# Kernel tuning notes

Measured on AMD Instinct MI355X. Metric: run time of the kernel, lower is better.

Reference implementation:

```python
import jax, jax.numpy as jnp
import numpy as np

S, B, D, E, F = 2048, 2, 1024, 8, 4096


def setup_inputs() -> dict:
    key = jax.random.key(0)
    ks = jax.random.split(key, 6)
    x = jax.random.normal(ks[0], (S, B, D), dtype=jnp.float32)
    w_switch = jax.random.normal(ks[1], (D, E), dtype=jnp.float32) / np.sqrt(D)
    b_switch = jnp.zeros((E,), dtype=jnp.float32)
    w1 = jax.random.normal(ks[2], (E, D, F), dtype=jnp.float32) / np.sqrt(D)
    b1 = jnp.zeros((E, F), dtype=jnp.float32)
    w2 = jax.random.normal(ks[3], (E, F, D), dtype=jnp.float32) / np.sqrt(F)
    b2 = jnp.zeros((E, D), dtype=jnp.float32)
    return {"x": x, "w_switch": w_switch, "b_switch": b_switch,
            "w1": w1, "b1": b1, "w2": w2, "b2": b2}


def reference(x, w_switch, b_switch, w1, b1, w2, b2):
    # x: [S, B, D] -> tokens [N, D]
    s, b, d = x.shape
    n_experts = w1.shape[0]
    xf = x.reshape(-1, d)                                    # [N, D]
    route_prob = jax.nn.softmax(xf @ w_switch + b_switch, axis=-1)  # [N, E]
    route_prob_max = jnp.max(route_prob, axis=-1)            # [N]
    routes = jnp.argmax(route_prob, axis=-1)                 # [N] int
    # is_scale_prob=True: scale token by its routing probability before FFN
    xs = xf * route_prob_max[:, None]                        # [N, D]
    # Per-expert FFN evaluated densely (drop_tokens=False => every token kept),
    # then each token selects its routed expert's output.
    h = jax.nn.relu(jnp.einsum('nd,edf->enf', xs, w1) + b1[:, None, :])  # [E, N, F]
    y = jnp.einsum('enf,efd->end', h, w2) + b2[:, None, :]               # [E, N, D]
    n = xf.shape[0]
    out = y[routes, jnp.arange(n)]                           # [N, D]
    counts = jnp.zeros((n_experts,), dtype=jnp.float32).at[routes].add(1.0)
    n_dropped = jnp.zeros((), dtype=jnp.int32)               # drop_tokens=False
    return out.reshape(s, b, d), counts, route_prob.sum(0), n_dropped
```

## Files before the change

### kernel.cpp

```cpp
#include <hip/hip_runtime.h>
#include <hip/hip_bf16.h>

#define NTOK 4096
#define DDIM 1024
#define NEXP 8
#define FDIM 4096

typedef __attribute__((ext_vector_type(4))) float f32x4;
typedef __attribute__((ext_vector_type(8))) short bf16x8;
typedef __attribute__((ext_vector_type(8))) unsigned short u16x8;

#define GLDS(g, l) __builtin_amdgcn_global_load_lds( \
    (const __attribute__((address_space(1))) unsigned int*)(g), \
    (__attribute__((address_space(3))) unsigned int*)(l), 16, 0, 0)

__global__ __launch_bounds__(256) void route_kernel(
    const float* __restrict__ x,
    const float* __restrict__ w_switch,
    const float* __restrict__ b_switch,
    __hip_bfloat16* __restrict__ xs,
    int* __restrict__ amax_arr,
    float* __restrict__ partial)
{
    const int tid = threadIdx.x;
    const int wave = tid >> 6, lane = tid & 63;
    __shared__ float pr[4][16];

    float wacc[16];
#pragma unroll
    for (int j = 0; j < 16; j++) wacc[j] = 0.0f;

    for (int i = 0; i < 4; i++) {
        const int n = blockIdx.x * 16 + wave * 4 + i;
        const float4* xr = (const float4*)(x + (size_t)n * DDIM);
        float4 xv[4];
#pragma unroll
        for (int j = 0; j < 4; j++) xv[j] = xr[lane + j * 64];

        float acc[NEXP];
#pragma unroll
        for (int e = 0; e < NEXP; e++) acc[e] = 0.0f;
#pragma unroll
        for (int j = 0; j < 4; j++) {
            const int dbase = (lane + j * 64) * 4;
#pragma unroll
            for (int c = 0; c < 4; c++) {
                const float4* wr = (const float4*)(w_switch + (size_t)(dbase + c) * NEXP);
                float4 w0 = wr[0], w1 = wr[1];
                float xvc = ((const float*)&xv[j])[c];
                acc[0] += xvc * w0.x; acc[1] += xvc * w0.y;
                acc[2] += xvc * w0.z; acc[3] += xvc * w0.w;
                acc[4] += xvc * w1.x; acc[5] += xvc * w1.y;
                acc[6] += xvc * w1.z; acc[7] += xvc * w1.w;
            }
        }
#pragma unroll
        for (int e = 0; e < NEXP; e++) {
            float v = acc[e];
#pragma unroll
            for (int off = 32; off > 0; off >>= 1) v += __shfl_xor(v, off, 64);
            acc[e] = v;
        }
        float mx = -1e30f;
#pragma unroll
        for (int e = 0; e < NEXP; e++) {
            acc[e] += b_switch[e];
            mx = fmaxf(mx, acc[e]);
        }
        float sum = 0.0f;
#pragma unroll
        for (int e = 0; e < NEXP; e++) { acc[e] = __expf(acc[e] - mx); sum += acc[e]; }
        float inv = 1.0f / sum;
        float pmax = -1.0f; int amax = 0;
#pragma unroll
        for (int e = 0; e < NEXP; e++) {
            float p = acc[e] * inv;
            acc[e] = p;
            if (p > pmax) { pmax = p; amax = e; }
        }
#pragma unroll
        for (int e = 0; e < NEXP; e++) {
            wacc[e] += acc[e];
            wacc[8 + e] += (amax == e) ? 1.0f : 0.0f;
        }
        if (lane == 0) amax_arr[n] = amax;
#pragma unroll
        for (int j = 0; j < 4; j++) {
            ushort4 pk;
            __hip_bfloat16* pp = (__hip_bfloat16*)&pk;
            pp[0] = __float2bfloat16(xv[j].x * pmax);
            pp[1] = __float2bfloat16(xv[j].y * pmax);
            pp[2] = __float2bfloat16(xv[j].z * pmax);
            pp[3] = __float2bfloat16(xv[j].w * pmax);
            *(ushort4*)(xs + (size_t)n * DDIM + (lane + j * 64) * 4) = pk;
        }
    }
    if (lane == 0) {
#pragma unroll
        for (int j = 0; j < 16; j++) pr[wave][j] = wacc[j];
    }
    __syncthreads();
    if (tid < 16)
        partial[blockIdx.x * 16 + tid] = pr[0][tid] + pr[1][tid] + pr[2][tid] + pr[3][tid];
}

__global__ __launch_bounds__(256) void finalize_kernel(
    const float* __restrict__ partial, float* __restrict__ out_tail)
{
    __shared__ float red[16][16];
    const int j = threadIdx.x & 15, g = threadIdx.x >> 4;
    float s = 0.0f;
    for (int k = 0; k < 16; k++) s += partial[(size_t)(g + k * 16) * 16 + j];
    red[g][j] = s;
    __syncthreads();
    if (threadIdx.x < 16) {
        float t = 0.0f;
        for (int k = 0; k < 16; k++) t += red[k][threadIdx.x];
        int dst = (threadIdx.x < 8) ? (8 + threadIdx.x) : (threadIdx.x - 8);
        out_tail[dst] = t;
    }
    if (threadIdx.x == 16) out_tail[16] = 0.0f;
}

__global__ __launch_bounds__(1024) void bucket_kernel(
    const int* __restrict__ amax_arr, int* __restrict__ bucket, int* __restrict__ ecnt)
{
    const int e = blockIdx.x;
    __shared__ int ctr;
    if (threadIdx.x == 0) ctr = 0;
    __syncthreads();
    const int lane = threadIdx.x & 63;
    for (int c = 0; c < NTOK; c += 1024) {
        int t = c + threadIdx.x;
        bool my = (amax_arr[t] == e);
        unsigned long long mask = __ballot(my);
        int cnt = __popcll(mask);
        int base = 0;
        if (lane == 0 && cnt) base = atomicAdd(&ctr, cnt);
        base = __shfl(base, 0, 64);
        if (my) {
            int rank = __popcll(mask & ((1ull << lane) - 1ull));
            bucket[e * NTOK + base + rank] = t;
        }
    }
    __syncthreads();
    if (threadIdx.x == 0) ecnt[e] = ctr;
}

template <int R, int C>
__global__ __launch_bounds__(256) void transpose_kernel(
    const float* __restrict__ in, __hip_bfloat16* __restrict__ outp)
{
    const int e = blockIdx.z;
    const int r0 = blockIdx.y * 64, c0 = blockIdx.x * 64;
    __shared__ __hip_bfloat16 t[64 * 65];
    const int tid = threadIdx.x;
    const int ri = tid >> 4, c4 = (tid & 15) * 4;
    const float* src = in + ((size_t)e * R + r0) * C + c0;
#pragma unroll
    for (int rr = 0; rr < 4; rr++) {
        int r = ri + rr * 16;
        float4 v = *(const float4*)(src + (size_t)r * C + c4);
        t[r * 65 + c4 + 0] = __float2bfloat16(v.x);
        t[r * 65 + c4 + 1] = __float2bfloat16(v.y);
        t[r * 65 + c4 + 2] = __float2bfloat16(v.z);
        t[r * 65 + c4 + 3] = __float2bfloat16(v.w);
    }
    __syncthreads();
    const int co = tid >> 2, m = tid & 3;
    u16x8 v0, v1;
#pragma unroll
    for (int idx = 0; idx < 8; idx++)
        ((unsigned short*)&v0)[idx] = *(const unsigned short*)&t[(m * 16 + idx) * 65 + co];
#pragma unroll
    for (int idx = 0; idx < 8; idx++)
        ((unsigned short*)&v1)[idx] = *(const unsigned short*)&t[(m * 16 + idx + 8) * 65 + co];
    __hip_bfloat16* dst = outp + ((size_t)e * C + c0 + co) * R + r0 + m * 16;
    *(u16x8*)(dst) = v0;
    *(u16x8*)(dst + 8) = v1;
}

template <int MODE, int K, int NN>
__global__ __launch_bounds__(256) void gemm_kernel(
    const __hip_bfloat16* __restrict__ A,
    const __hip_bfloat16* __restrict__ Bt,
    const float* __restrict__ bias,
    const int* __restrict__ bucket,
    const int* __restrict__ ecnt,
    void* __restrict__ Out)
{
    const int e = blockIdx.z;
    const int cnt = ecnt[e];
    const int m0 = blockIdx.y * 128;
    if (m0 >= cnt) return;
    const int n0 = blockIdx.x * 128;

    __shared__ __align__(16) __hip_bfloat16 Asm[128 * 32];
    __shared__ __align__(16) __hip_bfloat16 Bsm[128 * 32];
    __shared__ int toks[128];

    const int tid = threadIdx.x;
    if (tid < 128) {
        int r = m0 + tid;
        toks[tid] = bucket[e * NTOK + (r < cnt ? r : cnt - 1)];
    }
    __syncthreads();

    const int wave = tid >> 6, lane = tid & 63;
    const int r = lane & 15, kq = lane >> 4;
    const int g0 = 2 * wave, g1 = 2 * wave + 1;

    const __hip_bfloat16* pA0 = A + (size_t)toks[g0 * 16 + r] * K + kq * 8;
    const __hip_bfloat16* pA1 = A + (size_t)toks[g1 * 16 + r] * K + kq * 8;
    const __hip_bfloat16* pB0 = Bt + ((size_t)e * NN + n0 + g0 * 16 + r) * K + kq * 8;
    const __hip_bfloat16* pB1 = Bt + ((size_t)e * NN + n0 + g1 * 16 + r) * K + kq * 8;
    char* lA0 = (char*)Asm + g0 * 1024;
    char* lA1 = (char*)Asm + g1 * 1024;
    char* lB0 = (char*)Bsm + g0 * 1024;
    char* lB1 = (char*)Bsm + g1 * 1024;

    const int wm = wave & 1, wn = wave >> 1;
    f32x4 acc[4][4];
#pragma unroll
    for (int t = 0; t < 4; t++)
#pragma unroll
        for (int u = 0; u < 4; u++) acc[t][u] = (f32x4){0.f, 0.f, 0.f, 0.f};

    for (int k0 = 0; k0 < K; k0 += 32) {
        GLDS(pA0, lA0); GLDS(pA1, lA1);
        GLDS(pB0, lB0); GLDS(pB1, lB1);
        pA0 += 32; pA1 += 32; pB0 += 32; pB1 += 32;
        __syncthreads();
        bf16x8 a[4], b[4];
#pragma unroll
        for (int t = 0; t < 4; t++)
            a[t] = *(const bf16x8*)((const char*)Asm + (wm * 4 + t) * 1024 + lane * 16);
#pragma unroll
        for (int u = 0; u < 4; u++)
            b[u] = *(const bf16x8*)((const char*)Bsm + (wn * 4 + u) * 1024 + lane * 16);
#pragma unroll
        for (int t = 0; t < 4; t++)
#pragma unroll
            for (int u = 0; u < 4; u++)
                acc[t][u] = __builtin_amdgcn_mfma_f32_16x16x32_bf16(a[t], b[u], acc[t][u], 0, 0, 0);
        __syncthreads();
    }

    const int quad = lane >> 4, l15 = lane & 15;
    float bv[4];
#pragma unroll
    for (int u = 0; u < 4; u++)
        bv[u] = bias[(size_t)e * NN + n0 + wn * 64 + u * 16 + l15];
#pragma unroll
    for (int t = 0; t < 4; t++) {
#pragma unroll
        for (int rr = 0; rr < 4; rr++) {
            int row = wm * 64 + t * 16 + quad * 4 + rr;
            if (m0 + row < cnt) {
                int tok = toks[row];
#pragma unroll
                for (int u = 0; u < 4; u++) {
                    int col = n0 + wn * 64 + u * 16 + l15;
                    float v = acc[t][u][rr] + bv[u];
                    if (MODE == 0) {
                        v = fmaxf(v, 0.0f);
                        ((__hip_bfloat16*)Out)[(size_t)tok * NN + col] = __float2bfloat16(v);
                    } else {
                        ((float*)Out)[(size_t)tok * NN + col] = v;
                    }
                }
            }
        }
    }
}

extern "C" void kernel_launch(void* const* d_in, const int* in_sizes, int n_in,
                              void* d_out, int out_size, void* d_ws, size_t ws_size,
                              hipStream_t stream) {
    const float* x        = (const float*)d_in[0];
    const float* w_switch = (const float*)d_in[1];
    const float* b_switch = (const float*)d_in[2];
    const float* w1       = (const float*)d_in[3];
    const float* b1       = (const float*)d_in[4];
    const float* w2       = (const float*)d_in[5];
    const float* b2       = (const float*)d_in[6];

    float* out = (float*)d_out;
    float* out_tail = out + (size_t)NTOK * DDIM;

    char* ws = (char*)d_ws;
    __hip_bfloat16* xs = (__hip_bfloat16*)(ws);
    __hip_bfloat16* h  = (__hip_bfloat16*)(ws + 8388608ull);
    __hip_bfloat16* wt = (__hip_bfloat16*)(ws + 41943040ull);
    int* bucket        = (int*)(ws + 109051904ull);
    int* amax_arr      = (int*)(ws + 109182976ull);
    float* partial     = (float*)(ws + 109199360ull);
    int* ecnt          = (int*)(ws + 109215744ull);

    hipLaunchKernelGGL(route_kernel, dim3(256), dim3(256), 0, stream,
                       x, w_switch, b_switch, xs, amax_arr, partial);
    hipLaunchKernelGGL(finalize_kernel, dim3(1), dim3(256), 0, stream, partial, out_tail);
    hipLaunchKernelGGL(bucket_kernel, dim3(NEXP), dim3(1024), 0, stream,
                       amax_arr, bucket, ecnt);

    hipLaunchKernelGGL((transpose_kernel<DDIM, FDIM>), dim3(FDIM / 64, DDIM / 64, NEXP),
                       dim3(256), 0, stream, w1, wt);
    hipLaunchKernelGGL((gemm_kernel<0, DDIM, FDIM>), dim3(FDIM / 128, 32, NEXP),
                       dim3(256), 0, stream, xs, wt, b1, bucket, ecnt, (void*)h);

    hipLaunchKernelGGL((transpose_kernel<FDIM, DDIM>), dim3(DDIM / 64, FDIM / 64, NEXP),
                       dim3(256), 0, stream, w2, wt);
    hipLaunchKernelGGL((gemm_kernel<1, FDIM, DDIM>), dim3(DDIM / 128, 32, NEXP),
                       dim3(256), 0, stream, h, wt, b2, bucket, ecnt, (void*)out);
}
```

Baseline: 590.2 us.

## Compact expert tile table and split-K second FFN GEMM with atomic accumulation

Builds a compact table of (expert, row-tile) entries so the GEMM grids launch only as many blocks as there are real tiles, instead of 32 tiles per expert with most exiting early. The second GEMM is split along K into two halves whose partial sums are added atomically into an output that a new kernel pre-fills with the routed expert's bias. This gives the small-N second GEMM more parallelism, at the cost of atomic float traffic, an extra init pass over the output, and non-deterministic summation order.

```diff
diff --git a/kernel.cpp b/kernel.cpp
--- a/kernel.cpp
+++ b/kernel.cpp
@@ -5,6 +5,7 @@
 #define DDIM 1024
 #define NEXP 8
 #define FDIM 4096
+#define MAXTILES 40
 
 typedef __attribute__((ext_vector_type(4))) float f32x4;
 typedef __attribute__((ext_vector_type(8))) short bf16x8;
@@ -102,24 +103,6 @@
     __syncthreads();
     if (tid < 16)
         partial[blockIdx.x * 16 + tid] = pr[0][tid] + pr[1][tid] + pr[2][tid] + pr[3][tid];
-}
-
-__global__ __launch_bounds__(256) void finalize_kernel(
-    const float* __restrict__ partial, float* __restrict__ out_tail)
-{
-    __shared__ float red[16][16];
-    const int j = threadIdx.x & 15, g = threadIdx.x >> 4;
-    float s = 0.0f;
-    for (int k = 0; k < 16; k++) s += partial[(size_t)(g + k * 16) * 16 + j];
-    red[g][j] = s;
-    __syncthreads();
-    if (threadIdx.x < 16) {
-        float t = 0.0f;
-        for (int k = 0; k < 16; k++) t += red[k][threadIdx.x];
-        int dst = (threadIdx.x < 8) ? (8 + threadIdx.x) : (threadIdx.x - 8);
-        out_tail[dst] = t;
-    }
-    if (threadIdx.x == 16) out_tail[16] = 0.0f;
 }
 
 __global__ __launch_bounds__(1024) void bucket_kernel(
@@ -147,6 +130,43 @@
     if (threadIdx.x == 0) ecnt[e] = ctr;
 }
 
+__global__ __launch_bounds__(256) void finalize_table_kernel(
+    const float* __restrict__ partial, const int* __restrict__ ecnt,
+    float* __restrict__ out_tail, int* __restrict__ table)
+{
+    __shared__ float red[16][16];
+    const int j = threadIdx.x & 15, g = threadIdx.x >> 4;
+    float s = 0.0f;
+    for (int k = 0; k < 16; k++) s += partial[(size_t)(g + k * 16) * 16 + j];
+    red[g][j] = s;
+    __syncthreads();
+    if (threadIdx.x < 16) {
+        float t = 0.0f;
+        for (int k = 0; k < 16; k++) t += red[k][threadIdx.x];
+        int dst = (threadIdx.x < 8) ? (8 + threadIdx.x) : (threadIdx.x - 8);
+        out_tail[dst] = t;
+    }
+    if (threadIdx.x == 16) out_tail[16] = 0.0f;
+    if (threadIdx.x == 0) {
+        int idx = 0;
+        for (int e = 0; e < NEXP; e++) {
+            int cnt = ecnt[e];
+            for (int m0 = 0; m0 < cnt; m0 += 128) table[idx++] = (e << 16) | m0;
+        }
+        for (; idx < MAXTILES; idx++) table[idx] = -1;
+    }
+}
+
+__global__ __launch_bounds__(256) void init_out_kernel(
+    const float* __restrict__ b2, const int* __restrict__ amax_arr,
+    float* __restrict__ out)
+{
+    const int t = blockIdx.x;
+    const int e = amax_arr[t];
+    const float4* br = (const float4*)(b2 + (size_t)e * DDIM);
+    ((float4*)(out + (size_t)t * DDIM))[threadIdx.x] = br[threadIdx.x];
+}
+
 template <int R, int C>
 __global__ __launch_bounds__(256) void transpose_kernel(
     const float* __restrict__ in, __hip_bfloat16* __restrict__ outp)
@@ -180,20 +200,23 @@
     *(u16x8*)(dst + 8) = v1;
 }
 
-template <int MODE, int K, int NN>
-__global__ __launch_bounds__(256) void gemm_kernel(
+template <int MODE, int K, int NN, int KS>
+__device__ __forceinline__ void gemm_body(
     const __hip_bfloat16* __restrict__ A,
     const __hip_bfloat16* __restrict__ Bt,
     const float* __restrict__ bias,
     const int* __restrict__ bucket,
     const int* __restrict__ ecnt,
+    const int* __restrict__ table,
     void* __restrict__ Out)
 {
-    const int e = blockIdx.z;
+    const int entry = table[blockIdx.y];
+    if (entry < 0) return;
+    const int e = entry >> 16;
+    const int m0 = entry & 0xffff;
     const int cnt = ecnt[e];
-    const int m0 = blockIdx.y * 128;
-    if (m0 >= cnt) return;
     const int n0 = blockIdx.x * 128;
+    const int kbase = (K / KS) * blockIdx.z;
 
     __shared__ __align__(16) __hip_bfloat16 Asm[128 * 32];
     __shared__ __align__(16) __hip_bfloat16 Bsm[128 * 32];
@@ -210,10 +233,10 @@
     const int r = lane & 15, kq = lane >> 4;
     const int g0 = 2 * wave, g1 = 2 * wave + 1;
 
-    const __hip_bfloat16* pA0 = A + (size_t)toks[g0 * 16 + r] * K + kq * 8;
-    const __hip_bfloat16* pA1 = A + (size_t)toks[g1 * 16 + r] * K + kq * 8;
-    const __hip_bfloat16* pB0 = Bt + ((size_t)e * NN + n0 + g0 * 16 + r) * K + kq * 8;
-    const __hip_bfloat16* pB1 = Bt + ((size_t)e * NN + n0 + g1 * 16 + r) * K + kq * 8;
+    const __hip_bfloat16* pA0 = A + (size_t)toks[g0 * 16 + r] * K + kbase + kq * 8;
+    const __hip_bfloat16* pA1 = A + (size_t)toks[g1 * 16 + r] * K + kbase + kq * 8;
+    const __hip_bfloat16* pB0 = Bt + ((size_t)e * NN + n0 + g0 * 16 + r) * K + kbase + kq * 8;
+    const __hip_bfloat16* pB1 = Bt + ((size_t)e * NN + n0 + g1 * 16 + r) * K + kbase + kq * 8;
     char* lA0 = (char*)Asm + g0 * 1024;
     char* lA1 = (char*)Asm + g1 * 1024;
     char* lB0 = (char*)Bsm + g0 * 1024;
@@ -226,7 +249,7 @@
 #pragma unroll
         for (int u = 0; u < 4; u++) acc[t][u] = (f32x4){0.f, 0.f, 0.f, 0.f};
 
-    for (int k0 = 0; k0 < K; k0 += 32) {
+    for (int k0 = 0; k0 < K / KS; k0 += 32) {
         GLDS(pA0, lA0); GLDS(pA1, lA1);
         GLDS(pB0, lB0); GLDS(pB1, lB1);
         pA0 += 32; pA1 += 32; pB0 += 32; pB1 += 32;
@@ -250,7 +273,7 @@
     float bv[4];
 #pragma unroll
     for (int u = 0; u < 4; u++)
-        bv[u] = bias[(size_t)e * NN + n0 + wn * 64 + u * 16 + l15];
+        bv[u] = (MODE == 0) ? bias[(size_t)e * NN + n0 + wn * 64 + u * 16 + l15] : 0.0f;
 #pragma unroll
     for (int t = 0; t < 4; t++) {
 #pragma unroll
@@ -266,12 +289,28 @@
                         v = fmaxf(v, 0.0f);
                         ((__hip_bfloat16*)Out)[(size_t)tok * NN + col] = __float2bfloat16(v);
                     } else {
-                        ((float*)Out)[(size_t)tok * NN + col] = v;
+                        unsafeAtomicAdd(&((float*)Out)[(size_t)tok * NN + col], v);
                     }
                 }
             }
         }
     }
+}
+
+__global__ __launch_bounds__(256) void gemm_ffn1(
+    const __hip_bfloat16* __restrict__ A, const __hip_bfloat16* __restrict__ Bt,
+    const float* __restrict__ bias, const int* __restrict__ bucket,
+    const int* __restrict__ ecnt, const int* __restrict__ table, void* __restrict__ Out)
+{
+    gemm_body<0, DDIM, FDIM, 1>(A, Bt, bias, bucket, ecnt, table, Out);
+}
+
+__global__ __launch_bounds__(256) void gemm_ffn2(
+    const __hip_bfloat16* __restrict__ A, const __hip_bfloat16* __restrict__ Bt,
+    const float* __restrict__ bias, const int* __restrict__ bucket,
+    const int* __restrict__ ecnt, const int* __restrict__ table, void* __restrict__ Out)
+{
+    gemm_body<1, FDIM, DDIM, 2>(A, Bt, bias, bucket, ecnt, table, Out);
 }
 
 extern "C" void kernel_launch(void* const* d_in, const int* in_sizes, int n_in,
@@ -296,20 +335,24 @@
     int* amax_arr      = (int*)(ws + 109182976ull);
     float* partial     = (float*)(ws + 109199360ull);
     int* ecnt          = (int*)(ws + 109215744ull);
+    int* table         = (int*)(ws + 109215776ull);
 
     hipLaunchKernelGGL(route_kernel, dim3(256), dim3(256), 0, stream,
                        x, w_switch, b_switch, xs, amax_arr, partial);
-    hipLaunchKernelGGL(finalize_kernel, dim3(1), dim3(256), 0, stream, partial, out_tail);
     hipLaunchKernelGGL(bucket_kernel, dim3(NEXP), dim3(1024), 0, stream,
                        amax_arr, bucket, ecnt);
+    hipLaunchKernelGGL(finalize_table_kernel, dim3(1), dim3(256), 0, stream,
+                       partial, ecnt, out_tail, table);
+    hipLaunchKernelGGL(init_out_kernel, dim3(NTOK), dim3(256), 0, stream,
+                       b2, amax_arr, out);
 
     hipLaunchKernelGGL((transpose_kernel<DDIM, FDIM>), dim3(FDIM / 64, DDIM / 64, NEXP),
                        dim3(256), 0, stream, w1, wt);
-    hipLaunchKernelGGL((gemm_kernel<0, DDIM, FDIM>), dim3(FDIM / 128, 32, NEXP),
-                       dim3(256), 0, stream, xs, wt, b1, bucket, ecnt, (void*)h);
+    hipLaunchKernelGGL(gemm_ffn1, dim3(FDIM / 128, MAXTILES), dim3(256), 0, stream,
+                       xs, wt, b1, bucket, ecnt, table, (void*)h);
 
     hipLaunchKernelGGL((transpose_kernel<FDIM, DDIM>), dim3(DDIM / 64, FDIM / 64, NEXP),
                        dim3(256), 0, stream, w2, wt);
-    hipLaunchKernelGGL((gemm_kernel<1, FDIM, DDIM>), dim3(DDIM / 128, 32, NEXP),
-                       dim3(256), 0, stream, h, wt, b2, bucket, ecnt, (void*)out);
-}
+    hipLaunchKernelGGL(gemm_ffn2, dim3(DDIM / 128, MAXTILES, 2), dim3(256), 0, stream,
+                       h, wt, b2, bucket, ecnt, table, (void*)out);
+}
```

Result: faster. 529.5 us (-10.3%).
